# Performance work log

Hardware: AMD Instinct MI355X
Metric: run time of the kernel (lower is better)

Reference implementation:

```python
import jax, jax.numpy as jnp
import numpy as np


def _gru_scan(x_seq, Wih, Whh, bih, bhh):
    # x_seq: (S, N, D); PyTorch GRU/GRUCell gate math, h0 = 0. Returns (S, N, H).
    H = Whh.shape[1]
    gi_all = x_seq @ Wih.T + bih  # precompute input projections: (S, N, 3H)

    def step(h, gi):
        gh = h @ Whh.T + bhh
        ir, iz, inn = jnp.split(gi, 3, axis=-1)
        hr, hz, hn = jnp.split(gh, 3, axis=-1)
        r = jax.nn.sigmoid(ir + hr)
        z = jax.nn.sigmoid(iz + hz)
        n = jnp.tanh(inn + r * hn)
        h_new = (1.0 - z) * n + z * h
        return h_new, h_new

    h0 = jnp.zeros((x_seq.shape[1], H), x_seq.dtype)
    _, ys = jax.lax.scan(step, h0, gi_all)
    return ys


def setup_inputs() -> dict:
    key = jax.random.key(0)
    ks = jax.random.split(key, 40)
    B, T = 32, 800
    NOTE, E, P, H0, H1, FE, RE = 128, 256, 256, 512, 512, 64, 64

    def w(k, shape):
        return jax.random.normal(k, shape, dtype=jnp.float32) * 0.05

    return {
        "note": jax.random.randint(ks[0], (B, T), 0, NOTE, dtype=jnp.int64),
        "f0_prev": jax.random.normal(ks[1], (B, T), dtype=jnp.float32),
        "rmse_prev": jax.random.normal(ks[2], (B, T), dtype=jnp.float32),
        "note_emb": w(ks[3], (NOTE, E)),
        "f0_W": w(ks[4], (FE, 1)), "f0_b": w(ks[5], (FE,)),
        "rmse_W": w(ks[6], (RE, 1)), "rmse_b": w(ks[7], (RE,)),
        "pre1_W": w(ks[8], (P, E)), "pre1_b": w(ks[9], (P,)),
        "pre2_W": w(ks[10], (P, P)), "pre2_b": w(ks[11], (P,)),
        "encf_Wih": w(ks[12], (3 * H0, P)), "encf_Whh": w(ks[13], (3 * H0, H0)),
        "encf_bih": w(ks[14], (3 * H0,)), "encf_bhh": w(ks[15], (3 * H0,)),
        "encb_Wih": w(ks[16], (3 * H0, P)), "encb_Whh": w(ks[17], (3 * H0, H0)),
        "encb_bih": w(ks[18], (3 * H0,)), "encb_bhh": w(ks[19], (3 * H0,)),
        "decf_Wih": w(ks[20], (3 * H1, 2 * H0 + FE)), "decf_Whh": w(ks[21], (3 * H1, H1)),
        "decf_bih": w(ks[22], (3 * H1,)), "decf_bhh": w(ks[23], (3 * H1,)),
        "decr_Wih": w(ks[24], (3 * H1, 2 * H0 + RE)), "decr_Whh": w(ks[25], (3 * H1, H1)),
        "decr_bih": w(ks[26], (3 * H1,)), "decr_bhh": w(ks[27], (3 * H1,)),
        "postf_W": w(ks[28], (1, H1)), "postf_b": w(ks[29], (1,)),
        "postr_W": w(ks[30], (1, H1)), "postr_b": w(ks[31], (1,)),
    }


def reference(note, f0_prev, rmse_prev, note_emb, f0_W, f0_b, rmse_W, rmse_b,
              pre1_W, pre1_b, pre2_W, pre2_b,
              encf_Wih, encf_Whh, encf_bih, encf_bhh,
              encb_Wih, encb_Whh, encb_bih, encb_bhh,
              decf_Wih, decf_Whh, decf_bih, decf_bhh,
              decr_Wih, decr_Whh, decr_bih, decr_bhh,
              postf_W, postf_b, postr_W, postr_b):
    # Embeddings. Linear(1, FE) on a [B,T] signal == outer-broadcast with W[:,0].
    ne = note_emb[note]                                   # (B, T, E)
    f0e = f0_prev[..., None] * f0_W[:, 0] + f0_b          # (B, T, FE)
    rme = rmse_prev[..., None] * rmse_W[:, 0] + rmse_b    # (B, T, RE)

    # Prenet: Linear -> Tanh -> Linear -> Tanh
    h = jnp.tanh(jnp.tanh(ne @ pre1_W.T + pre1_b) @ pre2_W.T + pre2_b)  # (B, T, P)

    # Encoder: torch nn.GRU built WITHOUT batch_first and called with lengths=None,
    # so the recurrence runs over axis 0 (B) with T acting as the GRU batch. Replicated.
    ef = _gru_scan(h, encf_Wih, encf_Whh, encf_bih, encf_bhh)            # (B, T, H0)
    eb = _gru_scan(h[::-1], encb_Wih, encb_Whh, encb_bih, encb_bhh)[::-1]
    enc = jnp.concatenate([ef, eb], axis=-1)                             # (B, T, 2H0)

    # Decoders: GRUCell loop over T with teacher forcing (y_prevs has T>1 steps),
    # so step-t input is concat(enc[:, t], embed(prev[:, t])) -> standard scan.
    xt = jnp.transpose(enc, (1, 0, 2))                                   # (T, B, 2H0)
    hf = _gru_scan(jnp.concatenate([xt, jnp.transpose(f0e, (1, 0, 2))], -1),
                   decf_Wih, decf_Whh, decf_bih, decf_bhh)               # (T, B, H1)
    hr = _gru_scan(jnp.concatenate([xt, jnp.transpose(rme, (1, 0, 2))], -1),
                   decr_Wih, decr_Whh, decr_bih, decr_bhh)               # (T, B, H1)

    f0 = jnp.transpose((hf @ postf_W.T + postf_b)[..., 0], (1, 0))       # (B, T)
    rmse = jnp.transpose((hr @ postr_W.T + postr_b)[..., 0], (1, 0))     # (B, T)
    return (f0, rmse)
```

## Files before the change

kernel.cpp:

```cpp
#include <hip/hip_runtime.h>
#include <hip/hip_bf16.h>


typedef __bf16 bf16;
typedef bf16 bf16x8 __attribute__((ext_vector_type(8)));
typedef float f32x4 __attribute__((ext_vector_type(4)));
typedef float f32x2 __attribute__((ext_vector_type(2)));

#define BATCH 32
#define TLEN 800
#define BT (BATCH * TLEN)
#define WROW 768
#define WELEM 1179648

__device__ __forceinline__ float bf2f(bf16 v) {
    unsigned short u = __builtin_bit_cast(unsigned short, v);
    unsigned int x = ((unsigned int)u) << 16;
    return __builtin_bit_cast(float, x);
}
__device__ __forceinline__ bf16 f2bf(float f) {
    unsigned int x = __builtin_bit_cast(unsigned int, f);
    unsigned int r = (x + 0x7FFFu + ((x >> 16) & 1u)) >> 16;
    return __builtin_bit_cast(bf16, (unsigned short)r);
}
__device__ __forceinline__ bf16x8 ld8f(const float* p) {
    f32x4 a = *(const f32x4*)p;
    f32x4 b = *(const f32x4*)(p + 4);
    bf16x8 r;
#pragma unroll
    for (int i = 0; i < 4; i++) {
        r[i] = f2bf(a[i]);
        r[i + 4] = f2bf(b[i]);
    }
    return r;
}
__device__ __forceinline__ void splitv(f32x4 a, f32x4 b, bf16x8& vh, bf16x8& vl) {
#pragma unroll
    for (int j = 0; j < 4; j++) {
        bf16 h0 = f2bf(a[j]);
        vh[j] = h0;
        vl[j] = f2bf(a[j] - bf2f(h0));
        bf16 h1 = f2bf(b[j]);
        vh[j + 4] = h1;
        vl[j + 4] = f2bf(b[j] - bf2f(h1));
    }
}
__device__ __forceinline__ f32x4 mfma16(bf16x8 a, bf16x8 b, f32x4 c) {
    return __builtin_amdgcn_mfma_f32_16x16x32_bf16(a, b, c, 0, 0, 0);
}
__device__ __forceinline__ float sigm(float x) { return 1.f / (1.f + __expf(-x)); }

__device__ __forceinline__ void cst_f32(float* p, float v) {
    __hip_atomic_store((unsigned int*)p, __builtin_bit_cast(unsigned int, v),
                       __ATOMIC_RELAXED, __HIP_MEMORY_SCOPE_AGENT);
}
__device__ __forceinline__ float cld_f32(const float* p) {
    unsigned int u = __hip_atomic_load((const unsigned int*)p, __ATOMIC_RELAXED,
                                       __HIP_MEMORY_SCOPE_AGENT);
    return __builtin_bit_cast(float, u);
}
__device__ __forceinline__ f32x4 cld_f32x4(const float* p) {
    unsigned long long a = __hip_atomic_load((const unsigned long long*)p,
                                             __ATOMIC_RELAXED,
                                             __HIP_MEMORY_SCOPE_AGENT);
    unsigned long long b = __hip_atomic_load((const unsigned long long*)(p + 2),
                                             __ATOMIC_RELAXED,
                                             __HIP_MEMORY_SCOPE_AGENT);
    f32x2 fa = __builtin_bit_cast(f32x2, a);
    f32x2 fb = __builtin_bit_cast(f32x2, b);
    f32x4 r;
    r[0] = fa[0]; r[1] = fa[1]; r[2] = fb[0]; r[3] = fb[1];
    return r;
}

template <int MODE>
__global__ __launch_bounds__(256) void gemm01_k(
    const int* __restrict__ note, const float* __restrict__ asrc,
    const float* __restrict__ W, const float* __restrict__ bias,
    float* __restrict__ out, int t0, int TC) {
    __shared__ bf16 Ah[128][72], Al[128][72], Bs[128][72];

    const int tid = threadIdx.x;
    const int lane = tid & 63, wv = tid >> 6;
    const int wm = wv & 1, wn = wv >> 1;
    const int l15 = lane & 15, hi = lane >> 4;
    const int bm = blockIdx.x * 128, bn = blockIdx.y * 128;
    const int ch = (tid & 7) * 8, arow = tid >> 3;

    f32x4 acc[4][4] = {};
    const float* ap[4];
    if (MODE == 0) {
        int zc = 0;
        for (int i = 0; i < 64; i++) zc += (note[2 * i + 1] == 0) ? 1 : 0;
        const bool n64 = (zc >= 60);
#pragma unroll
        for (int i = 0; i < 4; i++) {
            int m = bm + arow + 32 * i;
            int b = m / TC, tt = m - b * TC;
            int idx = b * TLEN + t0 + tt;
            int id = n64 ? note[2 * idx] : note[idx];
            id = id < 0 ? 0 : (id > 127 ? 127 : id);
            ap[i] = asrc + (size_t)id * 256;
        }
    } else {
#pragma unroll
        for (int i = 0; i < 4; i++) ap[i] = asrc + (size_t)(bm + arow + 32 * i) * 256;
    }

    for (int k0 = 0; k0 < 256; k0 += 64) {
#pragma unroll
        for (int i = 0; i < 4; i++) {
            int row = arow + 32 * i;
            f32x4 va = *(const f32x4*)(ap[i] + k0 + ch);
            f32x4 vb = *(const f32x4*)(ap[i] + k0 + ch + 4);
            bf16x8 vh, vl;
            splitv(va, vb, vh, vl);
            *(bf16x8*)&Ah[row][ch] = vh;
            *(bf16x8*)&Al[row][ch] = vl;
        }
#pragma unroll
        for (int i = 0; i < 4; i++) {
            int row = arow + 32 * i;
            *(bf16x8*)&Bs[row][ch] = ld8f(W + (size_t)(bn + row) * 256 + k0 + ch);
        }
        __syncthreads();
#pragma unroll
        for (int kk = 0; kk < 64; kk += 32) {
            bf16x8 ah[4], al[4], bb[4];
#pragma unroll
            for (int mt = 0; mt < 4; mt++) {
                ah[mt] = *(const bf16x8*)&Ah[wm * 64 + mt * 16 + l15][kk + hi * 8];
                al[mt] = *(const bf16x8*)&Al[wm * 64 + mt * 16 + l15][kk + hi * 8];
            }
#pragma unroll
            for (int nt = 0; nt < 4; nt++)
                bb[nt] = *(const bf16x8*)&Bs[wn * 64 + nt * 16 + l15][kk + hi * 8];
#pragma unroll
            for (int mt = 0; mt < 4; mt++)
#pragma unroll
                for (int nt = 0; nt < 4; nt++) {
                    acc[mt][nt] = mfma16(ah[mt], bb[nt], acc[mt][nt]);
                    acc[mt][nt] = mfma16(al[mt], bb[nt], acc[mt][nt]);
                }
        }
        __syncthreads();
    }

#pragma unroll
    for (int mt = 0; mt < 4; mt++)
#pragma unroll
        for (int nt = 0; nt < 4; nt++) {
            int n = bn + wn * 64 + nt * 16 + l15;
            float bs = bias[n];
#pragma unroll
            for (int r = 0; r < 4; r++) {
                int m = bm + wm * 64 + mt * 16 + hi * 4 + r;
                out[(size_t)m * 256 + n] = tanhf(acc[mt][nt][r] + bs);
            }
        }
}

__global__ __launch_bounds__(256) void gemm2_k(
    const float* __restrict__ ef, const float* __restrict__ eb,
    const float* __restrict__ sig, const float* __restrict__ sigW,
    const float* __restrict__ sigB, const float* __restrict__ W,
    const float* __restrict__ bias, float* __restrict__ out, int t0, int TC) {
    __shared__ bf16 Ah[128][72], Al[128][72];
    __shared__ bf16 Bh[64][72], Bl[64][72];

    const int tid = threadIdx.x;
    const int lane = tid & 63, wv = tid >> 6;
    const int wm = wv & 1, wn = wv >> 1;
    const int l15 = lane & 15, hi = lane >> 4;
    const int bm = blockIdx.x * 128, bn = blockIdx.y * 64;
    const int ch = (tid & 7) * 8, arow = tid >> 3;

    f32x4 acc[4][2] = {};
    int rb[4];
    float sigv[4];
#pragma unroll
    for (int i = 0; i < 4; i++) {
        int m = bm + arow + 32 * i;
        int tt = m >> 5, b = m & 31;
        rb[i] = b * TC + tt;
        sigv[i] = sig[b * TLEN + t0 + tt];
    }

    for (int k0 = 0; k0 < 1088; k0 += 64) {
#pragma unroll
        for (int i = 0; i < 4; i++) {
            int row = arow + 32 * i;
            int k = k0 + ch;
            f32x4 va, vb;
            if (k < 512) {
                va = *(const f32x4*)(ef + (size_t)rb[i] * 512 + k);
                vb = *(const f32x4*)(ef + (size_t)rb[i] * 512 + k + 4);
            } else if (k < 1024) {
                va = *(const f32x4*)(eb + (size_t)rb[i] * 512 + (k - 512));
                vb = *(const f32x4*)(eb + (size_t)rb[i] * 512 + (k - 512) + 4);
            } else {
                f32x4 w0 = *(const f32x4*)(sigW + ch);
                f32x4 w1 = *(const f32x4*)(sigW + ch + 4);
                f32x4 b0 = *(const f32x4*)(sigB + ch);
                f32x4 b1 = *(const f32x4*)(sigB + ch + 4);
                float s = sigv[i];
#pragma unroll
                for (int j = 0; j < 4; j++) {
                    va[j] = s * w0[j] + b0[j];
                    vb[j] = s * w1[j] + b1[j];
                }
            }
            bf16x8 vh, vl;
            splitv(va, vb, vh, vl);
            *(bf16x8*)&Ah[row][ch] = vh;
            *(bf16x8*)&Al[row][ch] = vl;
        }
#pragma unroll
        for (int i = 0; i < 2; i++) {
            int row = arow + 32 * i;
            const float* src = W + (size_t)(bn + row) * 1088 + k0 + ch;
            f32x4 va = *(const f32x4*)src;
            f32x4 vb = *(const f32x4*)(src + 4);
            bf16x8 vh, vl;
            splitv(va, vb, vh, vl);
            *(bf16x8*)&Bh[row][ch] = vh;
            *(bf16x8*)&Bl[row][ch] = vl;
        }
        __syncthreads();
#pragma unroll
        for (int kk = 0; kk < 64; kk += 32) {
            bf16x8 ah[4], al[4], bh[2], bl[2];
#pragma unroll
            for (int mt = 0; mt < 4; mt++) {
                ah[mt] = *(const bf16x8*)&Ah[wm * 64 + mt * 16 + l15][kk + hi * 8];
                al[mt] = *(const bf16x8*)&Al[wm * 64 + mt * 16 + l15][kk + hi * 8];
            }
#pragma unroll
            for (int nt = 0; nt < 2; nt++) {
                bh[nt] = *(const bf16x8*)&Bh[wn * 32 + nt * 16 + l15][kk + hi * 8];
                bl[nt] = *(const bf16x8*)&Bl[wn * 32 + nt * 16 + l15][kk + hi * 8];
            }
#pragma unroll
            for (int mt = 0; mt < 4; mt++)
#pragma unroll
                for (int nt = 0; nt < 2; nt++) {
                    acc[mt][nt] = mfma16(ah[mt], bh[nt], acc[mt][nt]);
                    acc[mt][nt] = mfma16(al[mt], bh[nt], acc[mt][nt]);
                    acc[mt][nt] = mfma16(ah[mt], bl[nt], acc[mt][nt]);
                }
        }
        __syncthreads();
    }

#pragma unroll
    for (int mt = 0; mt < 4; mt++)
#pragma unroll
        for (int nt = 0; nt < 2; nt++) {
            int n = bn + wn * 32 + nt * 16 + l15;
            float bs = bias[n];
#pragma unroll
            for (int r = 0; r < 4; r++) {
                int m = bm + wm * 64 + mt * 16 + hi * 4 + r;
                out[(size_t)m * 1536 + n] = acc[mt][nt][r] + bs;
            }
        }
}

__global__ __launch_bounds__(256) void wsplit_k(
    const float* __restrict__ fWih, const float* __restrict__ fWhh,
    const float* __restrict__ bWih, const float* __restrict__ bWhh,
    bf16* __restrict__ out) {
    const int idx = (blockIdx.x * 256 + threadIdx.x) * 8;
    const int dir = blockIdx.y;
    const int row = idx / WROW, k = idx - row * WROW;
    const float* src = (k < 256)
                           ? ((dir ? bWih : fWih) + (size_t)row * 256 + k)
                           : ((dir ? bWhh : fWhh) + (size_t)row * 512 + (k - 256));
    bf16* oh = out + (size_t)dir * 2 * WELEM;
    bf16* ol = oh + WELEM;
    f32x4 a = *(const f32x4*)src;
    f32x4 b = *(const f32x4*)(src + 4);
    bf16x8 vh, vl;
    splitv(a, b, vh, vl);
    *(bf16x8*)(oh + idx) = vh;
    *(bf16x8*)(ol + idx) = vl;
}

__global__ __launch_bounds__(256) void enc_step_k(
    int step, int TC, const float* __restrict__ hpre, float* __restrict__ efb,
    float* __restrict__ ebb, const bf16* __restrict__ wsp,
    const float* __restrict__ fbih, const float* __restrict__ fbhh,
    const float* __restrict__ bbih, const float* __restrict__ bbhh) {
    __shared__ bf16 As[32][72], Alo[32][72];

    const int dir = blockIdx.z;
    const bf16* Wh = wsp + (size_t)dir * 2 * WELEM;
    const bf16* Wl = Wh + WELEM;
    const float* bih = dir ? bbih : fbih;
    const float* bhh = dir ? bbhh : fbhh;
    float* outb = dir ? ebb : efb;
    const int bsrc = dir ? (31 - step) : step;
    const int prevb = dir ? (32 - step) : (step - 1);

    const int tid = threadIdx.x;
    const int lane = tid & 63, wv = tid >> 6;
    const int mt = wv & 1, jt = wv >> 1;
    const int l15 = lane & 15, hi = lane >> 4;
    const int mtile = blockIdx.x, jtile = blockIdx.y;
    const int ch = (tid & 7) * 8, arow = tid >> 3;

    const int jrow = jtile * 32 + jt * 16 + l15;
    const bf16* Whr = Wh + (size_t)jrow * WROW;
    const bf16* Wlr = Wl + (size_t)jrow * WROW;
    const bf16* Whz = Wh + (size_t)(512 + jrow) * WROW;
    const bf16* Wlz = Wl + (size_t)(512 + jrow) * WROW;
    const bf16* Whn = Wh + (size_t)(1024 + jrow) * WROW;
    const bf16* Wln = Wl + (size_t)(1024 + jrow) * WROW;

    f32x4 acc_r = {}, acc_z = {}, acc_in = {}, acc_hn = {};

    const int nblocks = (step == 0) ? 4 : 12;
    for (int kb = 0; kb < nblocks; kb++) {
        int k0 = kb * 64;
        {
            int trow = mtile * 32 + arow;
            int tcl = trow < TC ? trow : TC - 1;
            const float* src = (k0 < 256)
                                   ? (hpre + ((size_t)bsrc * TC + tcl) * 256 + k0 + ch)
                                   : (outb + ((size_t)prevb * TC + tcl) * 512 + (k0 - 256) + ch);
            f32x4 va = *(const f32x4*)src;
            f32x4 vb = *(const f32x4*)(src + 4);
            bf16x8 vh, vl;
            splitv(va, vb, vh, vl);
            *(bf16x8*)&As[arow][ch] = vh;
            *(bf16x8*)&Alo[arow][ch] = vl;
        }
        __syncthreads();
#pragma unroll
        for (int kk = 0; kk < 64; kk += 32) {
            bf16x8 a = *(const bf16x8*)&As[mt * 16 + l15][kk + hi * 8];
            bf16x8 alo = *(const bf16x8*)&Alo[mt * 16 + l15][kk + hi * 8];
            const int ko = k0 + kk + hi * 8;
            bf16x8 brh = *(const bf16x8*)(Whr + ko);
            bf16x8 brl = *(const bf16x8*)(Wlr + ko);
            bf16x8 bzh = *(const bf16x8*)(Whz + ko);
            bf16x8 bzl = *(const bf16x8*)(Wlz + ko);
            bf16x8 bnh = *(const bf16x8*)(Whn + ko);
            bf16x8 bnl = *(const bf16x8*)(Wln + ko);
            acc_r = mfma16(a, brh, acc_r);
            acc_r = mfma16(alo, brh, acc_r);
            acc_r = mfma16(a, brl, acc_r);
            acc_z = mfma16(a, bzh, acc_z);
            acc_z = mfma16(alo, bzh, acc_z);
            acc_z = mfma16(a, bzl, acc_z);
            if (k0 < 256) {
                acc_in = mfma16(a, bnh, acc_in);
                acc_in = mfma16(alo, bnh, acc_in);
                acc_in = mfma16(a, bnl, acc_in);
            } else {
                acc_hn = mfma16(a, bnh, acc_hn);
                acc_hn = mfma16(alo, bnh, acc_hn);
                acc_hn = mfma16(a, bnl, acc_hn);
            }
        }
        __syncthreads();
    }

    int j = jrow;
    float bir = bih[j] + bhh[j];
    float biz = bih[512 + j] + bhh[512 + j];
    float bin = bih[1024 + j];
    float bhn = bhh[1024 + j];
#pragma unroll
    for (int r = 0; r < 4; r++) {
        int trow = mtile * 32 + mt * 16 + hi * 4 + r;
        if (trow < TC) {
            float rr = sigm(acc_r[r] + bir);
            float zz = sigm(acc_z[r] + biz);
            float nn = tanhf(acc_in[r] + bin + rr * (acc_hn[r] + bhn));
            float hp = (step > 0) ? outb[((size_t)prevb * TC + trow) * 512 + j] : 0.f;
            outb[((size_t)bsrc * TC + trow) * 512 + j] = (1.f - zz) * nn + zz * hp;
        }
    }
}

__global__ __launch_bounds__(256, 1) void dec_k(
    const float* __restrict__ giF, const float* __restrict__ giR,
    const float* __restrict__ WhhF, const float* __restrict__ WhhR,
    const float* __restrict__ bhhF, const float* __restrict__ bhhR,
    float* __restrict__ HcurF, float* __restrict__ HcurR,
    const float* __restrict__ HprevF, const float* __restrict__ HprevR,
    int* __restrict__ flags, int t0, int TC) {
    const int d = blockIdx.x >> 4;
    const int g = blockIdx.x & 15;
    const float* gi = d ? giR : giF;
    const float* Whh = d ? WhhR : WhhF;
    const float* bhh = d ? bhhR : bhhF;
    float* Hcur = d ? HcurR : HcurF;
    const float* Hprev = d ? HprevR : HprevF;
    int* flg = flags + d * 16;

    const int tid = threadIdx.x;
    const int lane = tid & 63, wv = tid >> 6;
    const int mt = wv & 1, jt = wv >> 1;
    const int l15 = lane & 15, hi = lane >> 4;
    const int j_abs = g * 32 + jt * 16 + l15;

    bf16x8 Wf[3][16];
#pragma unroll
    for (int s = 0; s < 3; s++)
#pragma unroll
        for (int kb = 0; kb < 16; kb++)
            Wf[s][kb] = ld8f(Whh + (size_t)(s * 512 + j_abs) * 512 + kb * 32 + hi * 8);

    const float bhr = bhh[j_abs];
    const float bhz = bhh[512 + j_abs];
    const float bhn = bhh[1024 + j_abs];

    float hpreg[4] = {0.f, 0.f, 0.f, 0.f};

    for (int tt = 0; tt < TC; tt++) {
        const int t = t0 + tt;
        float gr[4], gz[4], gn[4];
#pragma unroll
        for (int r = 0; r < 4; r++) {
            int b = mt * 16 + hi * 4 + r;
            const float* gp = gi + ((size_t)tt * BATCH + b) * 1536 + j_abs;
            gr[r] = gp[0];
            gz[r] = gp[512];
            gn[r] = gp[1024];
        }

        f32x4 ar = {}, az = {}, an = {};
        float hp[4] = {0.f, 0.f, 0.f, 0.f};
        if (t > 0) {
            const float* base;
            if (tt > 0) {
                if (wv == 0 && lane < 16) {
                    while (__hip_atomic_load(&flg[lane], __ATOMIC_RELAXED,
                                             __HIP_MEMORY_SCOPE_AGENT) < t)
                        __builtin_amdgcn_s_sleep(1);
                }
                __syncthreads();
                base = Hcur + (size_t)(tt - 1) * BATCH * 512;
            } else {
                base = Hprev + (size_t)(TC - 1) * BATCH * 512;
            }
            const float* ap = base + (size_t)(mt * 16 + l15) * 512 + hi * 8;
#pragma unroll
            for (int half = 0; half < 2; half++) {
                f32x4 raw[8][2];
#pragma unroll
                for (int q = 0; q < 8; q++) {
                    int kb = half * 8 + q;
                    raw[q][0] = cld_f32x4(ap + kb * 32);
                    raw[q][1] = cld_f32x4(ap + kb * 32 + 4);
                }
#pragma unroll
                for (int q = 0; q < 8; q++) {
                    int kb = half * 8 + q;
                    bf16x8 ah, al;
                    splitv(raw[q][0], raw[q][1], ah, al);
                    ar = mfma16(ah, Wf[0][kb], ar);
                    ar = mfma16(al, Wf[0][kb], ar);
                    az = mfma16(ah, Wf[1][kb], az);
                    az = mfma16(al, Wf[1][kb], az);
                    an = mfma16(ah, Wf[2][kb], an);
                    an = mfma16(al, Wf[2][kb], an);
                }
            }
            if (tt > 0) {
#pragma unroll
                for (int r = 0; r < 4; r++) hp[r] = hpreg[r];
            } else {
#pragma unroll
                for (int r = 0; r < 4; r++) {
                    int b = mt * 16 + hi * 4 + r;
                    hp[r] = cld_f32(base + (size_t)b * 512 + j_abs);
                }
            }
        }
#pragma unroll
        for (int r = 0; r < 4; r++) {
            int b = mt * 16 + hi * 4 + r;
            float rr = sigm(gr[r] + ar[r] + bhr);
            float zz = sigm(gz[r] + az[r] + bhz);
            float nn = tanhf(gn[r] + rr * (an[r] + bhn));
            float hnew = (1.f - zz) * nn + zz * hp[r];
            cst_f32(&Hcur[((size_t)tt * BATCH + b) * 512 + j_abs], hnew);
            hpreg[r] = hnew;
        }
        __syncthreads();
        if (tid == 0)
            __hip_atomic_store(&flg[g], t + 1, __ATOMIC_RELAXED,
                               __HIP_MEMORY_SCOPE_AGENT);
    }
}

__global__ __launch_bounds__(256) void post_k(
    const float* __restrict__ H, const float* __restrict__ W,
    const float* __restrict__ bs, float* __restrict__ out, int t0) {
    const int wv = threadIdx.x >> 6, lane = threadIdx.x & 63;
    const int row = blockIdx.x * 4 + wv;
    const int tt = row >> 5, b = row & 31;
    const float bias = bs[0];
    const float* hp = H + (size_t)row * 512 + lane * 8;
    f32x4 h0 = *(const f32x4*)hp;
    f32x4 h1 = *(const f32x4*)(hp + 4);
    f32x4 w0 = *(const f32x4*)(W + lane * 8);
    f32x4 w1 = *(const f32x4*)(W + lane * 8 + 4);
    float s = 0.f;
#pragma unroll
    for (int i = 0; i < 4; i++) s += h0[i] * w0[i] + h1[i] * w1[i];
#pragma unroll
    for (int off = 32; off > 0; off >>= 1) s += __shfl_down(s, off);
    if (lane == 0) out[b * TLEN + t0 + tt] = s + bias;
}

__global__ void zero_k(int* __restrict__ flags) {
    int i = blockIdx.x * 256 + threadIdx.x;
    if (i < 2 * TLEN)
        __hip_atomic_store(&flags[i], 0, __ATOMIC_RELAXED,
                           __HIP_MEMORY_SCOPE_AGENT);
}

extern "C" void kernel_launch(void* const* d_in, const int* in_sizes, int n_in,
                              void* d_out, int out_size, void* d_ws, size_t ws_size,
                              hipStream_t stream) {
    const int* note = (const int*)d_in[0];
    const float* f0_prev = (const float*)d_in[1];
    const float* rmse_prev = (const float*)d_in[2];
    const float* note_emb = (const float*)d_in[3];
    const float* f0_W = (const float*)d_in[4];
    const float* f0_b = (const float*)d_in[5];
    const float* rmse_W = (const float*)d_in[6];
    const float* rmse_b = (const float*)d_in[7];
    const float* pre1_W = (const float*)d_in[8];
    const float* pre1_b = (const float*)d_in[9];
    const float* pre2_W = (const float*)d_in[10];
    const float* pre2_b = (const float*)d_in[11];
    const float* encf_Wih = (const float*)d_in[12];
    const float* encf_Whh = (const float*)d_in[13];
    const float* encf_bih = (const float*)d_in[14];
    const float* encf_bhh = (const float*)d_in[15];
    const float* encb_Wih = (const float*)d_in[16];
    const float* encb_Whh = (const float*)d_in[17];
    const float* encb_bih = (const float*)d_in[18];
    const float* encb_bhh = (const float*)d_in[19];
    const float* decf_Wih = (const float*)d_in[20];
    const float* decf_Whh = (const float*)d_in[21];
    const float* decf_bih = (const float*)d_in[22];
    const float* decf_bhh = (const float*)d_in[23];
    const float* decr_Wih = (const float*)d_in[24];
    const float* decr_Whh = (const float*)d_in[25];
    const float* decr_bih = (const float*)d_in[26];
    const float* decr_bhh = (const float*)d_in[27];
    const float* postf_W = (const float*)d_in[28];
    const float* postf_b = (const float*)d_in[29];
    const float* postr_W = (const float*)d_in[30];
    const float* postr_b = (const float*)d_in[31];
    float* out = (float*)d_out;

    const size_t WSPB = (size_t)4 * WELEM * 2;
    const int tcs[9] = {800, 400, 200, 100, 80, 40, 20, 8, 4};
    int TC = 4;
    for (int i = 0; i < 9; i++) {
        int tc = tcs[i];
        int slots = (tc == TLEN) ? 1 : 2;
        size_t need = (size_t)(2 * 65536 + 2 * 196608 + 2 * slots * 65536) * tc +
                      WSPB + 131072;
        if (ws_size >= need) { TC = tc; break; }
    }
    const int NC = TLEN / TC;
    const int slots = (NC == 1) ? 1 : 2;

    char* ws = (char*)d_ws;
    size_t off = 0;
    auto carve = [&](size_t bytes) {
        void* p = ws + off;
        off += (bytes + 255) & ~(size_t)255;
        return p;
    };
    const size_t slotB = (size_t)65536 * TC;
    float* ef_c = (float*)carve(slotB);
    float* eb_c = (float*)carve(slotB);
    float* giF_c = (float*)carve((size_t)196608 * TC);
    float* giR_c = (float*)carve((size_t)196608 * TC);
    float* ringF = (float*)carve(slotB * slots);
    float* ringR = (float*)carve(slotB * slots);
    bf16* wsp = (bf16*)carve(WSPB);
    int* flags = (int*)carve(2 * TLEN * 4);
    float* t1_c = giF_c;
    float* hpre_c = giF_c + (size_t)8192 * TC;

    zero_k<<<dim3(7), 256, 0, stream>>>(flags);
    wsplit_k<<<dim3(576, 2), 256, 0, stream>>>(encf_Wih, encf_Whh, encb_Wih,
                                               encb_Whh, wsp);

    const size_t slotE = (size_t)TC * BATCH * 512;

    for (int c = 0; c < NC; c++) {
        const int t0 = c * TC;
        const int mg = TC * 32 / 128;

        gemm01_k<0><<<dim3(mg, 2), 256, 0, stream>>>(note, note_emb, pre1_W, pre1_b,
                                                     t1_c, t0, TC);
        gemm01_k<1><<<dim3(mg, 2), 256, 0, stream>>>(nullptr, t1_c, pre2_W, pre2_b,
                                                     hpre_c, t0, TC);
        const int etiles = (TC + 31) / 32;
        for (int i = 0; i < 32; i++)
            enc_step_k<<<dim3(etiles, 16, 2), 256, 0, stream>>>(
                i, TC, hpre_c, ef_c, eb_c, wsp, encf_bih, encf_bhh, encb_bih,
                encb_bhh);

        gemm2_k<<<dim3(mg, 24), 256, 0, stream>>>(ef_c, eb_c, f0_prev, f0_W, f0_b,
                                                  decf_Wih, decf_bih, giF_c, t0, TC);
        gemm2_k<<<dim3(mg, 24), 256, 0, stream>>>(ef_c, eb_c, rmse_prev, rmse_W,
                                                  rmse_b, decr_Wih, decr_bih, giR_c,
                                                  t0, TC);

        float* HcurF = ringF + (size_t)(c & (slots - 1)) * slotE;
        const float* HprevF = ringF + (size_t)((c - 1) & (slots - 1)) * slotE;
        float* HcurR = ringR + (size_t)(c & (slots - 1)) * slotE;
        const float* HprevR = ringR + (size_t)((c - 1) & (slots - 1)) * slotE;

        dec_k<<<dim3(32), 256, 0, stream>>>(giF_c, giR_c, decf_Whh, decr_Whh,
                                            decf_bhh, decr_bhh, HcurF, HcurR,
                                            HprevF, HprevR, flags, t0, TC);

        post_k<<<dim3(TC * 32 / 4), 256, 0, stream>>>(HcurF, postf_W, postf_b,
                                                      out, t0);
        post_k<<<dim3(TC * 32 / 4), 256, 0, stream>>>(HcurR, postr_W, postr_b,
                                                      out + BT, t0);
    }
    (void)in_sizes; (void)n_in; (void)out_size; (void)ws_size;
}
```

Baseline: 12.88 ms.

## Double-buffer encoder weight/activation tiles in LDS and split decoder blocks by batch half

The encoder step kernel now stages both the activation tile and the bf16 hi/lo weight tiles through double-buffered shared memory. It prefetches the next K-block into registers while the current one is computed, which removes one barrier per iteration and replaces strided per-lane global weight loads with coalesced ones. The decoder kernel changes its block mapping so each block covers 64 hidden units for one half of the batch. Each block then waits only on the 8 flags of its own batch half, which shrinks cross-block dependencies. The cost is more LDS use and more registers held for the prefetch, and the decoder flag layout grows to 32 flags per direction, so the host must allocate and reset them to match.

Result: faster. 11.10 ms (-13.8%).

```diff
diff --git a/kernel.cpp b/kernel.cpp
--- a/kernel.cpp
+++ b/kernel.cpp
@@ -291,11 +291,12 @@
     float* __restrict__ ebb, const bf16* __restrict__ wsp,
     const float* __restrict__ fbih, const float* __restrict__ fbhh,
     const float* __restrict__ bbih, const float* __restrict__ bbhh) {
-    __shared__ bf16 As[32][72], Alo[32][72];
+    __shared__ bf16 As[2][32][72], Alo[2][32][72];
+    __shared__ bf16 Bs[2][96][72], Blo[2][96][72];
 
     const int dir = blockIdx.z;
-    const bf16* Wh = wsp + (size_t)dir * 2 * WELEM;
-    const bf16* Wl = Wh + WELEM;
+    const bf16* Whi = wsp + (size_t)dir * 2 * WELEM;
+    const bf16* Wlg = Whi + WELEM;
     const float* bih = dir ? bbih : fbih;
     const float* bhh = dir ? bbhh : fbhh;
     float* outb = dir ? ebb : efb;
@@ -309,44 +310,82 @@
     const int mtile = blockIdx.x, jtile = blockIdx.y;
     const int ch = (tid & 7) * 8, arow = tid >> 3;
 
-    const int jrow = jtile * 32 + jt * 16 + l15;
-    const bf16* Whr = Wh + (size_t)jrow * WROW;
-    const bf16* Wlr = Wl + (size_t)jrow * WROW;
-    const bf16* Whz = Wh + (size_t)(512 + jrow) * WROW;
-    const bf16* Wlz = Wl + (size_t)(512 + jrow) * WROW;
-    const bf16* Whn = Wh + (size_t)(1024 + jrow) * WROW;
-    const bf16* Wln = Wl + (size_t)(1024 + jrow) * WROW;
+    const int trow = mtile * 32 + arow;
+    const int tcl = trow < TC ? trow : TC - 1;
+    const float* aph = hpre + ((size_t)bsrc * TC + tcl) * 256;
+    const float* apo = outb + ((size_t)prevb * TC + tcl) * 512;
+
+    int bro[3], bkc[3];
+    size_t bsr[3];
+#pragma unroll
+    for (int i = 0; i < 3; i++) {
+        int v = tid + 256 * i;
+        bro[i] = v >> 3;
+        bkc[i] = (v & 7) * 8;
+        bsr[i] = (size_t)((bro[i] >> 5) * 512 + jtile * 32 + (bro[i] & 31)) * WROW +
+                 bkc[i];
+    }
+
+    const int nblocks = (step == 0) ? 4 : 12;
 
     f32x4 acc_r = {}, acc_z = {}, acc_in = {}, acc_hn = {};
 
-    const int nblocks = (step == 0) ? 4 : 12;
+    f32x4 vaC = *(const f32x4*)(aph + ch);
+    f32x4 vbC = *(const f32x4*)(aph + ch + 4);
+    bf16x8 bhC0 = *(const bf16x8*)(Whi + bsr[0]);
+    bf16x8 bhC1 = *(const bf16x8*)(Whi + bsr[1]);
+    bf16x8 bhC2 = *(const bf16x8*)(Whi + bsr[2]);
+    bf16x8 blC0 = *(const bf16x8*)(Wlg + bsr[0]);
+    bf16x8 blC1 = *(const bf16x8*)(Wlg + bsr[1]);
+    bf16x8 blC2 = *(const bf16x8*)(Wlg + bsr[2]);
+
     for (int kb = 0; kb < nblocks; kb++) {
-        int k0 = kb * 64;
+        const int buf = kb & 1;
+        const int k0 = kb * 64;
+
+        f32x4 vaN = {}, vbN = {};
+        bf16x8 bhN0 = {}, bhN1 = {}, bhN2 = {}, blN0 = {}, blN1 = {}, blN2 = {};
+        if (kb + 1 < nblocks) {
+            int k0n = k0 + 64;
+            const float* asrc =
+                (k0n < 256) ? (aph + k0n + ch) : (apo + (k0n - 256) + ch);
+            vaN = *(const f32x4*)asrc;
+            vbN = *(const f32x4*)(asrc + 4);
+            bhN0 = *(const bf16x8*)(Whi + bsr[0] + k0n);
+            bhN1 = *(const bf16x8*)(Whi + bsr[1] + k0n);
+            bhN2 = *(const bf16x8*)(Whi + bsr[2] + k0n);
+            blN0 = *(const bf16x8*)(Wlg + bsr[0] + k0n);
+            blN1 = *(const bf16x8*)(Wlg + bsr[1] + k0n);
+            blN2 = *(const bf16x8*)(Wlg + bsr[2] + k0n);
+        }
+
         {
-            int trow = mtile * 32 + arow;
-            int tcl = trow < TC ? trow : TC - 1;
-            const float* src = (k0 < 256)
-                                   ? (hpre + ((size_t)bsrc * TC + tcl) * 256 + k0 + ch)
-                                   : (outb + ((size_t)prevb * TC + tcl) * 512 + (k0 - 256) + ch);
-            f32x4 va = *(const f32x4*)src;
-            f32x4 vb = *(const f32x4*)(src + 4);
             bf16x8 vh, vl;
-            splitv(va, vb, vh, vl);
-            *(bf16x8*)&As[arow][ch] = vh;
-            *(bf16x8*)&Alo[arow][ch] = vl;
-        }
-        __syncthreads();
+            splitv(vaC, vbC, vh, vl);
+            *(bf16x8*)&As[buf][arow][ch] = vh;
+            *(bf16x8*)&Alo[buf][arow][ch] = vl;
+            *(bf16x8*)&Bs[buf][bro[0]][bkc[0]] = bhC0;
+            *(bf16x8*)&Bs[buf][bro[1]][bkc[1]] = bhC1;
+            *(bf16x8*)&Bs[buf][bro[2]][bkc[2]] = bhC2;
+            *(bf16x8*)&Blo[buf][bro[0]][bkc[0]] = blC0;
+            *(bf16x8*)&Blo[buf][bro[1]][bkc[1]] = blC1;
+            *(bf16x8*)&Blo[buf][bro[2]][bkc[2]] = blC2;
+        }
+        __builtin_amdgcn_sched_barrier(0);
+        asm volatile("s_waitcnt lgkmcnt(0)" ::: "memory");
+        __builtin_amdgcn_s_barrier();
+        __builtin_amdgcn_sched_barrier(0);
+
 #pragma unroll
         for (int kk = 0; kk < 64; kk += 32) {
-            bf16x8 a = *(const bf16x8*)&As[mt * 16 + l15][kk + hi * 8];
-            bf16x8 alo = *(const bf16x8*)&Alo[mt * 16 + l15][kk + hi * 8];
-            const int ko = k0 + kk + hi * 8;
-            bf16x8 brh = *(const bf16x8*)(Whr + ko);
-            bf16x8 brl = *(const bf16x8*)(Wlr + ko);
-            bf16x8 bzh = *(const bf16x8*)(Whz + ko);
-            bf16x8 bzl = *(const bf16x8*)(Wlz + ko);
-            bf16x8 bnh = *(const bf16x8*)(Whn + ko);
-            bf16x8 bnl = *(const bf16x8*)(Wln + ko);
+            bf16x8 a = *(const bf16x8*)&As[buf][mt * 16 + l15][kk + hi * 8];
+            bf16x8 alo = *(const bf16x8*)&Alo[buf][mt * 16 + l15][kk + hi * 8];
+            bf16x8 brh = *(const bf16x8*)&Bs[buf][jt * 16 + l15][kk + hi * 8];
+            bf16x8 brl = *(const bf16x8*)&Blo[buf][jt * 16 + l15][kk + hi * 8];
+            bf16x8 bzh = *(const bf16x8*)&Bs[buf][32 + jt * 16 + l15][kk + hi * 8];
+            bf16x8 bzl = *(const bf16x8*)&Blo[buf][32 + jt * 16 + l15][kk + hi * 8];
+            bf16x8 bnh = *(const bf16x8*)&Bs[buf][64 + jt * 16 + l15][kk + hi * 8];
+            bf16x8 bnl = *(const bf16x8*)&Blo[buf][64 + jt * 16 + l15][kk + hi * 8];
             acc_r = mfma16(a, brh, acc_r);
             acc_r = mfma16(alo, brh, acc_r);
             acc_r = mfma16(a, brl, acc_r);
@@ -363,23 +402,26 @@
                 acc_hn = mfma16(a, bnl, acc_hn);
             }
         }
-        __syncthreads();
-    }
-
-    int j = jrow;
+
+        vaC = vaN; vbC = vbN;
+        bhC0 = bhN0; bhC1 = bhN1; bhC2 = bhN2;
+        blC0 = blN0; blC1 = blN1; blC2 = blN2;
+    }
+
+    int j = jtile * 32 + jt * 16 + l15;
     float bir = bih[j] + bhh[j];
     float biz = bih[512 + j] + bhh[512 + j];
     float bin = bih[1024 + j];
     float bhn = bhh[1024 + j];
 #pragma unroll
     for (int r = 0; r < 4; r++) {
-        int trow = mtile * 32 + mt * 16 + hi * 4 + r;
-        if (trow < TC) {
+        int trw = mtile * 32 + mt * 16 + hi * 4 + r;
+        if (trw < TC) {
             float rr = sigm(acc_r[r] + bir);
             float zz = sigm(acc_z[r] + biz);
             float nn = tanhf(acc_in[r] + bin + rr * (acc_hn[r] + bhn));
-            float hp = (step > 0) ? outb[((size_t)prevb * TC + trow) * 512 + j] : 0.f;
-            outb[((size_t)bsrc * TC + trow) * 512 + j] = (1.f - zz) * nn + zz * hp;
+            float hp = (step > 0) ? outb[((size_t)prevb * TC + trw) * 512 + j] : 0.f;
+            outb[((size_t)bsrc * TC + trw) * 512 + j] = (1.f - zz) * nn + zz * hp;
         }
     }
 }
@@ -392,19 +434,20 @@
     const float* __restrict__ HprevF, const float* __restrict__ HprevR,
     int* __restrict__ flags, int t0, int TC) {
     const int d = blockIdx.x >> 4;
-    const int g = blockIdx.x & 15;
+    const int c = (blockIdx.x >> 3) & 1;
+    const int g = blockIdx.x & 7;
     const float* gi = d ? giR : giF;
     const float* Whh = d ? WhhR : WhhF;
     const float* bhh = d ? bhhR : bhhF;
     float* Hcur = d ? HcurR : HcurF;
     const float* Hprev = d ? HprevR : HprevF;
-    int* flg = flags + d * 16;
+    int* flg = flags + d * 32 + c * 8;
 
     const int tid = threadIdx.x;
     const int lane = tid & 63, wv = tid >> 6;
-    const int mt = wv & 1, jt = wv >> 1;
     const int l15 = lane & 15, hi = lane >> 4;
-    const int j_abs = g * 32 + jt * 16 + l15;
+    const int j_abs = g * 64 + wv * 16 + l15;
+    const int brow = c * 16;
 
     bf16x8 Wf[3][16];
 #pragma unroll
@@ -424,7 +467,7 @@
         float gr[4], gz[4], gn[4];
 #pragma unroll
         for (int r = 0; r < 4; r++) {
-            int b = mt * 16 + hi * 4 + r;
+            int b = brow + hi * 4 + r;
             const float* gp = gi + ((size_t)tt * BATCH + b) * 1536 + j_abs;
             gr[r] = gp[0];
             gz[r] = gp[512];
@@ -436,7 +479,7 @@
         if (t > 0) {
             const float* base;
             if (tt > 0) {
-                if (wv == 0 && lane < 16) {
+                if (wv == 0 && lane < 8) {
                     while (__hip_atomic_load(&flg[lane], __ATOMIC_RELAXED,
                                              __HIP_MEMORY_SCOPE_AGENT) < t)
                         __builtin_amdgcn_s_sleep(1);
@@ -446,7 +489,7 @@
             } else {
                 base = Hprev + (size_t)(TC - 1) * BATCH * 512;
             }
-            const float* ap = base + (size_t)(mt * 16 + l15) * 512 + hi * 8;
+            const float* ap = base + (size_t)(brow + l15) * 512 + hi * 8;
 #pragma unroll
             for (int half = 0; half < 2; half++) {
                 f32x4 raw[8][2];
@@ -475,14 +518,14 @@
             } else {
 #pragma unroll
                 for (int r = 0; r < 4; r++) {
-                    int b = mt * 16 + hi * 4 + r;
+                    int b = brow + hi * 4 + r;
                     hp[r] = cld_f32(base + (size_t)b * 512 + j_abs);
                 }
             }
         }
 #pragma unroll
         for (int r = 0; r < 4; r++) {
-            int b = mt * 16 + hi * 4 + r;
+            int b = brow + hi * 4 + r;
             float rr = sigm(gr[r] + ar[r] + bhr);
             float zz = sigm(gz[r] + az[r] + bhz);
             float nn = tanhf(gn[r] + rr * (an[r] + bhn));
```
